# Performance work log

Hardware: AMD Instinct MI355X
Metric: run time of the kernel (lower is better)

Reference implementation:

```python
import jax, jax.numpy as jnp
import numpy as np

N = 100000   # num_nodes
E = 1600000  # num_edges
IN, HID, OUT = 128, 128, 64  # in_ft, 2*out_ft, out_ft


def setup_inputs() -> dict:
    key = jax.random.key(0)
    ks = jax.random.split(key, 8)
    x = jax.random.normal(ks[0], (N, IN), dtype=jnp.float32)
    edge_index = jax.random.randint(ks[1], (2, E), 0, N, dtype=jnp.int32)
    # Glorot-style init for GCNConv linear weights
    W1 = jax.random.normal(ks[2], (IN, HID), dtype=jnp.float32) / np.sqrt(IN).astype(np.float32)
    b1 = jnp.zeros((HID,), dtype=jnp.float32)
    W2 = jax.random.normal(ks[3], (HID, OUT), dtype=jnp.float32) / np.sqrt(HID).astype(np.float32)
    b2 = jnp.zeros((OUT,), dtype=jnp.float32)
    a = jnp.array([0.25], dtype=jnp.float32)  # shared PReLU slope (nn.PReLU default)
    return {"x": x, "edge_index": edge_index, "W1": W1, "b1": b1, "W2": W2, "b2": b2, "a": a}


def reference(x, edge_index, W1, b1, W2, b2, a):
    # PyG GCNConv semantics: add self-loops, symmetric normalization
    # norm_e = deg(src)^-1/2 * deg(dst)^-1/2, out[dst] += norm_e * (x @ W)[src] + bias
    src, dst = edge_index[0], edge_index[1]
    loops = jnp.arange(N, dtype=src.dtype)
    s = jnp.concatenate([src, loops])  # [E+N]
    d = jnp.concatenate([dst, loops])  # [E+N]
    deg = jax.ops.segment_sum(jnp.ones_like(d, dtype=x.dtype), d, num_segments=N)
    dis = jax.lax.rsqrt(deg)  # deg >= 1 thanks to self-loops
    norm = (dis[s] * dis[d])[:, None]  # [E+N, 1]

    def gcn_conv(h, W, b):
        hw = h @ W                                   # dense transform [N, F_out]
        msgs = hw[s] * norm                          # gather + scale  [E+N, F_out]
        return jax.ops.segment_sum(msgs, d, num_segments=N) + b  # scatter-add

    prelu = lambda v: jnp.where(v >= 0, v, a * v)

    h = prelu(gcn_conv(x, W1, b1))   # dropout p=0.0 -> identity
    return prelu(gcn_conv(h, W2, b2))
```

## Files before the change

### kernel.cpp

```cpp
#include <hip/hip_runtime.h>

#define N_NODES 100000
#define N_EDGES 1600000
#define BSH 9
#define NB  196
#define EPB 4096
#define CAPSH 14
#define GB  ((N_EDGES + EPB - 1) / EPB)
#define GG  ((N_NODES + 127) / 128)

typedef short bf16x8 __attribute__((ext_vector_type(8)));
typedef float f32x4 __attribute__((ext_vector_type(4)));
typedef float f32x2 __attribute__((ext_vector_type(2)));


__device__ __forceinline__ unsigned pack_bf16x2(float a, float b) {
    unsigned ua = __float_as_uint(a), ub = __float_as_uint(b);
    unsigned ra = (ua + 0x7fffu + ((ua >> 16) & 1u)) >> 16;
    unsigned rb = (ub + 0x7fffu + ((ub >> 16) & 1u)) >> 16;
    return ra | (rb << 16);
}
__device__ __forceinline__ unsigned short bf16_rne(float f) {
    unsigned u = __float_as_uint(f);
    return (unsigned short)((u + 0x7fffu + ((u >> 16) & 1u)) >> 16);
}
__device__ __forceinline__ f32x2 unpk(unsigned u) {
    f32x2 r;
    r.x = __uint_as_float(u << 16);
    r.y = __uint_as_float(u & 0xffff0000u);
    return r;
}


__device__ __forceinline__ void wt_body(const float* W, unsigned short* Wt, int C, int bid) {
    int t = bid * 256 + threadIdx.x;
    if (t >= 128 * C) return;
    int k = t / C, c = t % C;
    int g = k >> 3, j = k & 7;
    Wt[c * 128 + ((g ^ (c & 7)) << 3) + j] = bf16_rne(W[t]);
}

__global__ void setup_k(const float* __restrict__ W1, unsigned short* __restrict__ Wt1,
                        const float* __restrict__ W2, unsigned short* __restrict__ Wt2,
                        int* __restrict__ cursor) {
    int b = blockIdx.x;
    if (b < 64) { wt_body(W1, Wt1, 128, b); }
    else if (b < 96) { wt_body(W2, Wt2, 64, b - 64); }
    else {
        int t = threadIdx.x;
        if (t < NB) cursor[t] = t << CAPSH;
    }
}


__global__ __launch_bounds__(256) void bin_gemm1_k(
        const int* __restrict__ src, const int* __restrict__ dst,
        int* __restrict__ cursor, unsigned* __restrict__ binned,
        const float* __restrict__ X, const unsigned short* __restrict__ Wt,
        unsigned short* __restrict__ Y) {
    __shared__ int lhist[256];
    __shared__ int lcur[256];
    __shared__ short lds_w[128 * 128];
    int tid = threadIdx.x;

    if (blockIdx.x < GB) {
        lhist[tid] = 0;
        __syncthreads();
        int e0 = blockIdx.x * EPB;
#pragma unroll
        for (int i = 0; i < EPB / 256; ++i) {
            int e = e0 + i * 256 + tid;
            if (e < N_EDGES) atomicAdd(&lhist[dst[e] >> BSH], 1);
        }
        __syncthreads();
        {
            int c = lhist[tid];
            lcur[tid] = (tid < NB && c > 0) ? atomicAdd(&cursor[tid], c) : 0;
        }
        __syncthreads();
#pragma unroll
        for (int i = 0; i < EPB / 256; ++i) {
            int e = e0 + i * 256 + tid;
            if (e < N_EDGES) {
                int d = dst[e];
                int b = d >> BSH;
                int pos = atomicAdd(&lcur[b], 1);
                if (pos < ((b + 1) << CAPSH))
                    binned[pos] = ((unsigned)(d & ((1 << BSH) - 1)) << 17) | (unsigned)src[e];
            }
        }
        return;
    }

    {
        const uint4* srcp = (const uint4*)Wt;
        uint4* dstp = (uint4*)lds_w;
        for (int i = tid; i < 128 * 16; i += 256) dstp[i] = srcp[i];
    }
    __syncthreads();
    int lane = tid & 63;
    int r16 = lane & 15, kq = lane >> 4;
    int rbase = (blockIdx.x - GB) * 128 + (tid >> 6) * 32;
    f32x4 acc[2][8] = {};
#pragma unroll
    for (int kk = 0; kk < 4; ++kk) {
        int k0 = kk * 32 + kq * 8;
        bf16x8 a[2];
#pragma unroll
        for (int rt = 0; rt < 2; ++rt) {
            int row = rbase + rt * 16 + r16;
            if (row < N_NODES) {
                const float* xp = X + (size_t)row * 128 + k0;
                float4 f0 = *(const float4*)xp;
                float4 f1 = *(const float4*)(xp + 4);
                uint4 uu = make_uint4(pack_bf16x2(f0.x, f0.y), pack_bf16x2(f0.z, f0.w),
                                      pack_bf16x2(f1.x, f1.y), pack_bf16x2(f1.z, f1.w));
                a[rt] = *(bf16x8*)&uu;
            } else {
                bf16x8 z = {0, 0, 0, 0, 0, 0, 0, 0};
                a[rt] = z;
            }
        }
#pragma unroll
        for (int c = 0; c < 8; ++c) {
            int col = c * 16 + r16;
            int gp = (kk * 4 + kq) ^ (col & 7);
            bf16x8 b = *(const bf16x8*)&lds_w[col * 128 + gp * 8];
            acc[0][c] = __builtin_amdgcn_mfma_f32_16x16x32_bf16(a[0], b, acc[0][c], 0, 0, 0);
            acc[1][c] = __builtin_amdgcn_mfma_f32_16x16x32_bf16(a[1], b, acc[1][c], 0, 0, 0);
        }
    }
#pragma unroll
    for (int rt = 0; rt < 2; ++rt) {
#pragma unroll
        for (int c = 0; c < 8; ++c) {
#pragma unroll
            for (int r = 0; r < 4; ++r) {
                int row = rbase + rt * 16 + kq * 4 + r;
                if (row < N_NODES)
                    Y[(size_t)row * 128 + c * 16 + r16] = bf16_rne(acc[rt][c][r]);
            }
        }
    }
}

__global__ void bucket_scan_k(const int* __restrict__ cursor, int* __restrict__ bucket_base) {
    __shared__ int s[256];
    int tid = threadIdx.x;
    int v = (tid < NB) ? (cursor[tid] - (tid << CAPSH)) : 0;
    s[tid] = v; __syncthreads();
    for (int off = 1; off < 256; off <<= 1) {
        int t = 0;
        if (tid >= off) t = s[tid - off];
        __syncthreads();
        s[tid] += t;
        __syncthreads();
    }
    if (tid < NB) bucket_base[tid] = s[tid] - v;
}

__global__ __launch_bounds__(256) void deg_dis_k(const unsigned* __restrict__ binned,
                                                 const int* __restrict__ cursor,
                                                 const int* __restrict__ bucket_base,
                                                 int* __restrict__ row_start,
                                                 float* __restrict__ dis, int n, int E) {
    __shared__ int lcnt[1 << BSH];
    __shared__ int ls[256];
    int b = blockIdx.x, tid = threadIdx.x;
    for (int j = tid; j < (1 << BSH); j += 256) lcnt[j] = 0;
    __syncthreads();
    int base = b << CAPSH;
    int total = cursor[b] - base;
    for (int i = tid; i < total; i += 256)
        atomicAdd(&lcnt[binned[base + i] >> 17], 1);
    __syncthreads();
    int v0 = lcnt[2 * tid], v1 = lcnt[2 * tid + 1];
    int sv = v0 + v1;
    ls[tid] = sv;
    __syncthreads();
    for (int off = 1; off < 256; off <<= 1) {
        int t = 0;
        if (tid >= off) t = ls[tid - off];
        __syncthreads();
        ls[tid] += t;
        __syncthreads();
    }
    int pre = ls[tid] - sv;
    int nbase = b << BSH;
    int bb = bucket_base[b];
    int node0 = nbase + 2 * tid, node1 = node0 + 1;
    if (node0 < n) {
        row_start[node0] = bb + pre;
        dis[node0] = rsqrtf((float)(v0 + 1));
    }
    if (node1 < n) {
        row_start[node1] = bb + pre + v0;
        dis[node1] = rsqrtf((float)(v1 + 1));
    }
    if (b == NB - 1 && tid == 255) row_start[n] = E;
}

__global__ __launch_bounds__(256) void csr_k(const unsigned* __restrict__ binned,
                                             const int* __restrict__ cursor,
                                             const int* __restrict__ row_start,
                                             const float* __restrict__ dis,
                                             uint2* __restrict__ edge, int n) {
    __shared__ int lfill[1 << BSH];
    int b = blockIdx.x, tid = threadIdx.x;
    int nbase = b << BSH;
    for (int j = tid; j < (1 << BSH); j += 256) {
        int node = nbase + j;
        lfill[j] = (node < n) ? row_start[node] : 0;
    }
    __syncthreads();
    int base = b << CAPSH;
    int total = cursor[b] - base;
    for (int i = base + tid; i < base + total; i += 256) {
        unsigned u = binned[i];
        int s = u & 0x1FFFFu;
        int dl = u >> 17;
        int pos = atomicAdd(&lfill[dl], 1);
        edge[pos] = make_uint2((unsigned)s, __float_as_uint(dis[s] * dis[nbase + dl]));
    }
}


__global__ __launch_bounds__(256) void gemm2_k(const unsigned short* __restrict__ Xv,
                                               const unsigned short* __restrict__ Wt,
                                               unsigned short* __restrict__ Y, int nrows) {
    __shared__ short lds_w[64 * 128];
    int tid = threadIdx.x;
    {
        const uint4* srcp = (const uint4*)Wt;
        uint4* dstp = (uint4*)lds_w;
        for (int i = tid; i < 64 * 16; i += 256) dstp[i] = srcp[i];
    }
    __syncthreads();
    int lane = tid & 63;
    int r16 = lane & 15, kq = lane >> 4;
    int rbase = blockIdx.x * 128 + (tid >> 6) * 32;
    f32x4 acc[2][4] = {};
#pragma unroll
    for (int kk = 0; kk < 4; ++kk) {
        int k0 = kk * 32 + kq * 8;
        bf16x8 a[2];
#pragma unroll
        for (int rt = 0; rt < 2; ++rt) {
            int row = rbase + rt * 16 + r16;
            if (row < nrows) {
                a[rt] = *(const bf16x8*)(Xv + (size_t)row * 128 + k0);
            } else {
                bf16x8 z = {0, 0, 0, 0, 0, 0, 0, 0};
                a[rt] = z;
            }
        }
#pragma unroll
        for (int c = 0; c < 4; ++c) {
            int col = c * 16 + r16;
            int gp = (kk * 4 + kq) ^ (col & 7);
            bf16x8 b = *(const bf16x8*)&lds_w[col * 128 + gp * 8];
            acc[0][c] = __builtin_amdgcn_mfma_f32_16x16x32_bf16(a[0], b, acc[0][c], 0, 0, 0);
            acc[1][c] = __builtin_amdgcn_mfma_f32_16x16x32_bf16(a[1], b, acc[1][c], 0, 0, 0);
        }
    }
#pragma unroll
    for (int rt = 0; rt < 2; ++rt) {
#pragma unroll
        for (int c = 0; c < 4; ++c) {
#pragma unroll
            for (int r = 0; r < 4; ++r) {
                int row = rbase + rt * 16 + kq * 4 + r;
                if (row < nrows)
                    Y[(size_t)row * 64 + c * 16 + r16] = bf16_rne(acc[rt][c][r]);
            }
        }
    }
}


__global__ void agg1_k(const unsigned* __restrict__ hw, const int* __restrict__ row_start,
                       const uint2* __restrict__ edge, const float* __restrict__ dis,
                       const float* __restrict__ bias, const float* __restrict__ aslope,
                       unsigned* __restrict__ out, int n) {
    int w = (blockIdx.x * 256 + threadIdx.x) >> 6;
    int lane = threadIdx.x & 63;
    int g = lane >> 4;
    unsigned li = lane & 15;
    int node = w * 4 + g;
    bool valid = node < n;
    int e0 = valid ? row_start[node] : 0;
    int e1 = valid ? row_start[node + 1] : 0;
    unsigned rowoff = li << 4;
    const char* hwb = (const char*)hw;
    const char* edb = (const char*)edge;
    f32x2 acc[4] = {};
    int e = e0;
    while (__any(e < e1)) {
        if (e < e1) {
            uint2 ed[4];
            uint4 v[4];
#pragma unroll
            for (int u = 0; u < 4; ++u) {
                int ee = e + u;
                unsigned ec = (unsigned)((ee < e1) ? ee : (e1 - 1));
                ed[u] = *(const uint2*)(edb + (ec << 3));
            }
#pragma unroll
            for (int u = 0; u < 4; ++u)
                v[u] = *(const uint4*)(hwb + ((ed[u].x << 8) | rowoff));
#pragma unroll
            for (int u = 0; u < 4; ++u) {
                float nr = (e + u < e1) ? __uint_as_float(ed[u].y) : 0.f;
                f32x2 nr2 = {nr, nr};
                acc[0] += unpk(v[u].x) * nr2;
                acc[1] += unpk(v[u].y) * nr2;
                acc[2] += unpk(v[u].z) * nr2;
                acc[3] += unpk(v[u].w) * nr2;
            }
        }
        e += 4;
    }
    if (valid) {
        float dn = dis[node];
        f32x2 sw2 = {dn * dn, dn * dn};
        uint4 v = *(const uint4*)(hwb + (((unsigned)node << 8) | rowoff));
        acc[0] += unpk(v.x) * sw2;
        acc[1] += unpk(v.y) * sw2;
        acc[2] += unpk(v.z) * sw2;
        acc[3] += unpk(v.w) * sw2;
        float4 b0 = ((const float4*)bias)[li * 2];
        float4 b1 = ((const float4*)bias)[li * 2 + 1];
        float al = aslope[0];
        float r[8] = {acc[0].x + b0.x, acc[0].y + b0.y, acc[1].x + b0.z, acc[1].y + b0.w,
                      acc[2].x + b1.x, acc[2].y + b1.y, acc[3].x + b1.z, acc[3].y + b1.w};
#pragma unroll
        for (int j = 0; j < 8; ++j) r[j] = (r[j] >= 0.f) ? r[j] : al * r[j];
        uint4 o = make_uint4(pack_bf16x2(r[0], r[1]), pack_bf16x2(r[2], r[3]),
                             pack_bf16x2(r[4], r[5]), pack_bf16x2(r[6], r[7]));
        *(uint4*)(out + (size_t)node * 64 + li * 4) = o;
    }
}

__global__ void agg2_k(const unsigned* __restrict__ hw, const int* __restrict__ row_start,
                       const uint2* __restrict__ edge, const float* __restrict__ dis,
                       const float* __restrict__ bias, const float* __restrict__ aslope,
                       float* __restrict__ out, int n) {
    int w = (blockIdx.x * 256 + threadIdx.x) >> 6;
    int lane = threadIdx.x & 63;
    int g = lane >> 4;
    unsigned li = lane & 15;
    int node = w * 4 + g;
    bool valid = node < n;
    int e0 = valid ? row_start[node] : 0;
    int e1 = valid ? row_start[node + 1] : 0;
    unsigned rowoff = li << 3;
    const char* hwb = (const char*)hw;
    const char* edb = (const char*)edge;
    f32x2 acc[2] = {};
    int e = e0;
    while (__any(e < e1)) {
        if (e < e1) {
            uint2 ed[4];
            uint2 v[4];
#pragma unroll
            for (int u = 0; u < 4; ++u) {
                int ee = e + u;
                unsigned ec = (unsigned)((ee < e1) ? ee : (e1 - 1));
                ed[u] = *(const uint2*)(edb + (ec << 3));
            }
#pragma unroll
            for (int u = 0; u < 4; ++u)
                v[u] = *(const uint2*)(hwb + ((ed[u].x << 7) | rowoff));
#pragma unroll
            for (int u = 0; u < 4; ++u) {
                float nr = (e + u < e1) ? __uint_as_float(ed[u].y) : 0.f;
                f32x2 nr2 = {nr, nr};
                acc[0] += unpk(v[u].x) * nr2;
                acc[1] += unpk(v[u].y) * nr2;
            }
        }
        e += 4;
    }
    if (valid) {
        float dn = dis[node];
        f32x2 sw2 = {dn * dn, dn * dn};
        uint2 v = *(const uint2*)(hwb + (((unsigned)node << 7) | rowoff));
        acc[0] += unpk(v.x) * sw2;
        acc[1] += unpk(v.y) * sw2;
        float4 b = ((const float4*)bias)[li];
        float al = aslope[0];
        float r[4] = {acc[0].x + b.x, acc[0].y + b.y, acc[1].x + b.z, acc[1].y + b.w};
#pragma unroll
        for (int j = 0; j < 4; ++j) r[j] = (r[j] >= 0.f) ? r[j] : al * r[j];
        *(float4*)(out + (size_t)node * 64 + li * 4) = make_float4(r[0], r[1], r[2], r[3]);
    }
}


extern "C" void kernel_launch(void* const* d_in, const int* in_sizes, int n_in,
                              void* d_out, int out_size, void* d_ws, size_t ws_size,
                              hipStream_t stream) {
    const float* x  = (const float*)d_in[0];
    const int*   ei = (const int*)d_in[1];
    const int*   src = ei;
    const int*   dst = ei + N_EDGES;
    const float* W1 = (const float*)d_in[2];
    const float* b1 = (const float*)d_in[3];
    const float* W2 = (const float*)d_in[4];
    const float* b2 = (const float*)d_in[5];
    const float* a  = (const float*)d_in[6];
    float* out = (float*)d_out;

    char* ws = (char*)d_ws;
    size_t off = 0;
    auto alloc = [&](size_t bytes) -> void* {
        void* p = ws + off;
        off += (bytes + 255) & ~(size_t)255;
        return p;
    };
    int*            row_start = (int*)alloc((size_t)(N_NODES + 1) * 4);
    float*          dis       = (float*)alloc((size_t)N_NODES * 4);
    int*            cursor    = (int*)alloc(NB * 4);
    int*            bbase     = (int*)alloc(NB * 4);
    unsigned*       binned    = (unsigned*)alloc((size_t)NB * (1 << CAPSH) * 4);
    uint2*          edge      = (uint2*)alloc((size_t)N_EDGES * 8);
    unsigned*       hw1       = (unsigned*)alloc((size_t)N_NODES * 64 * 4);
    unsigned*       hbuf      = (unsigned*)alloc((size_t)N_NODES * 64 * 4);
    unsigned*       hw2       = (unsigned*)alloc((size_t)N_NODES * 32 * 4);
    unsigned short* Wt1       = (unsigned short*)alloc(128 * 128 * 2);
    unsigned short* Wt2       = (unsigned short*)alloc(64 * 128 * 2);

    setup_k<<<97, 256, 0, stream>>>(W1, Wt1, W2, Wt2, cursor);
    bin_gemm1_k<<<GB + GG, 256, 0, stream>>>(src, dst, cursor, binned,
                                             x, Wt1, (unsigned short*)hw1);
    bucket_scan_k<<<1, 256, 0, stream>>>(cursor, bbase);
    deg_dis_k<<<NB, 256, 0, stream>>>(binned, cursor, bbase, row_start, dis, N_NODES, N_EDGES);
    csr_k<<<NB, 256, 0, stream>>>(binned, cursor, row_start, dis, edge, N_NODES);

    int gA = (N_NODES + 1023) / 1024;
    gA = (N_NODES / 4 + 3) / 4;

    agg1_k<<<6250, 256, 0, stream>>>(hw1, row_start, edge, dis, b1, a, hbuf, N_NODES);
    gemm2_k<<<GG, 256, 0, stream>>>((unsigned short*)hbuf, Wt2, (unsigned short*)hw2, N_NODES);
    agg2_k<<<6250, 256, 0, stream>>>(hw2, row_start, edge, dis, b2, a, out, N_NODES);
    (void)gA;
}
```

Measured before the change: 186.4 us.

## Fuse layer-1 aggregation with second GEMM via LDS, unroll gathers by eight

```diff
diff --git a/kernel.cpp b/kernel.cpp
--- a/kernel.cpp
+++ b/kernel.cpp
@@ -8,6 +8,7 @@
 #define CAPSH 14
 #define GB  ((N_EDGES + EPB - 1) / EPB)
 #define GG  ((N_NODES + 127) / 128)
+#define AGB ((N_NODES + 63) / 64)
 
 typedef short bf16x8 __attribute__((ext_vector_type(8)));
 typedef float f32x4 __attribute__((ext_vector_type(4)));
@@ -225,121 +226,109 @@
 }
 
 
-__global__ __launch_bounds__(256) void gemm2_k(const unsigned short* __restrict__ Xv,
-                                               const unsigned short* __restrict__ Wt,
-                                               unsigned short* __restrict__ Y, int nrows) {
+__global__ __launch_bounds__(256) void agg1_gemm2_k(
+        const unsigned* __restrict__ hw, const int* __restrict__ row_start,
+        const uint2* __restrict__ edge, const float* __restrict__ dis,
+        const float* __restrict__ bias, const float* __restrict__ aslope,
+        const unsigned short* __restrict__ Wt2, unsigned short* __restrict__ hw2, int n) {
     __shared__ short lds_w[64 * 128];
+    __shared__ short lds_h[64 * 128];
     int tid = threadIdx.x;
     {
-        const uint4* srcp = (const uint4*)Wt;
+        const uint4* srcp = (const uint4*)Wt2;
         uint4* dstp = (uint4*)lds_w;
         for (int i = tid; i < 64 * 16; i += 256) dstp[i] = srcp[i];
     }
-    __syncthreads();
     int lane = tid & 63;
+    int g = lane >> 4;
+    unsigned li = lane & 15;
+    int wv = tid >> 6;
+    int nb0 = blockIdx.x * 64;
+    const char* hwb = (const char*)hw;
+    const char* edb = (const char*)edge;
+    float al = aslope[0];
+    float4 bb0 = ((const float4*)bias)[li * 2];
+    float4 bb1 = ((const float4*)bias)[li * 2 + 1];
+    unsigned rowoff = li << 4;
+#pragma unroll
+    for (int pass = 0; pass < 4; ++pass) {
+        int node = nb0 + wv * 16 + pass * 4 + g;
+        bool valid = node < n;
+        int e0 = valid ? row_start[node] : 0;
+        int e1 = valid ? row_start[node + 1] : 0;
+        f32x2 acc[4] = {};
+        int e = e0;
+        while (__any(e < e1)) {
+            if (e < e1) {
+                uint2 ed[8];
+                uint4 v[8];
+#pragma unroll
+                for (int u = 0; u < 8; ++u) {
+                    int ee = e + u;
+                    unsigned ec = (unsigned)((ee < e1) ? ee : (e1 - 1));
+                    ed[u] = *(const uint2*)(edb + (ec << 3));
+                }
+#pragma unroll
+                for (int u = 0; u < 8; ++u)
+                    v[u] = *(const uint4*)(hwb + ((ed[u].x << 8) | rowoff));
+#pragma unroll
+                for (int u = 0; u < 8; ++u) {
+                    float nr = (e + u < e1) ? __uint_as_float(ed[u].y) : 0.f;
+                    f32x2 nr2 = {nr, nr};
+                    acc[0] += unpk(v[u].x) * nr2;
+                    acc[1] += unpk(v[u].y) * nr2;
+                    acc[2] += unpk(v[u].z) * nr2;
+                    acc[3] += unpk(v[u].w) * nr2;
+                }
+            }
+            e += 8;
+        }
+        if (valid) {
+            float dn = dis[node];
+            f32x2 sw2 = {dn * dn, dn * dn};
+            uint4 v = *(const uint4*)(hwb + (((unsigned)node << 8) | rowoff));
+            acc[0] += unpk(v.x) * sw2;
+            acc[1] += unpk(v.y) * sw2;
+            acc[2] += unpk(v.z) * sw2;
+            acc[3] += unpk(v.w) * sw2;
+            float r[8] = {acc[0].x + bb0.x, acc[0].y + bb0.y, acc[1].x + bb0.z, acc[1].y + bb0.w,
+                          acc[2].x + bb1.x, acc[2].y + bb1.y, acc[3].x + bb1.z, acc[3].y + bb1.w};
+#pragma unroll
+            for (int j = 0; j < 8; ++j) r[j] = (r[j] >= 0.f) ? r[j] : al * r[j];
+            uint4 o = make_uint4(pack_bf16x2(r[0], r[1]), pack_bf16x2(r[2], r[3]),
+                                 pack_bf16x2(r[4], r[5]), pack_bf16x2(r[6], r[7]));
+            int lrow = node - nb0;
+            *(uint4*)((char*)lds_h + lrow * 256 + ((li ^ (unsigned)(lrow & 7)) << 4)) = o;
+        }
+    }
+    __syncthreads();
     int r16 = lane & 15, kq = lane >> 4;
-    int rbase = blockIdx.x * 128 + (tid >> 6) * 32;
-    f32x4 acc[2][4] = {};
+    int lrbase = wv * 16;
+    f32x4 acc[4] = {};
 #pragma unroll
     for (int kk = 0; kk < 4; ++kk) {
-        int k0 = kk * 32 + kq * 8;
-        bf16x8 a[2];
-#pragma unroll
-        for (int rt = 0; rt < 2; ++rt) {
-            int row = rbase + rt * 16 + r16;
-            if (row < nrows) {
-                a[rt] = *(const bf16x8*)(Xv + (size_t)row * 128 + k0);
-            } else {
-                bf16x8 z = {0, 0, 0, 0, 0, 0, 0, 0};
-                a[rt] = z;
-            }
-        }
+        int gA = kk * 4 + kq;
+        int lrow = lrbase + r16;
+        bf16x8 a = *(const bf16x8*)((const char*)lds_h + lrow * 256 + ((gA ^ (lrow & 7)) << 4));
 #pragma unroll
         for (int c = 0; c < 4; ++c) {
             int col = c * 16 + r16;
             int gp = (kk * 4 + kq) ^ (col & 7);
             bf16x8 b = *(const bf16x8*)&lds_w[col * 128 + gp * 8];
-            acc[0][c] = __builtin_amdgcn_mfma_f32_16x16x32_bf16(a[0], b, acc[0][c], 0, 0, 0);
-            acc[1][c] = __builtin_amdgcn_mfma_f32_16x16x32_bf16(a[1], b, acc[1][c], 0, 0, 0);
-        }
-    }
-#pragma unroll
-    for (int rt = 0; rt < 2; ++rt) {
-#pragma unroll
-        for (int c = 0; c < 4; ++c) {
-#pragma unroll
-            for (int r = 0; r < 4; ++r) {
-                int row = rbase + rt * 16 + kq * 4 + r;
-                if (row < nrows)
-                    Y[(size_t)row * 64 + c * 16 + r16] = bf16_rne(acc[rt][c][r]);
-            }
-        }
-    }
-}
-
-
-__global__ void agg1_k(const unsigned* __restrict__ hw, const int* __restrict__ row_start,
-                       const uint2* __restrict__ edge, const float* __restrict__ dis,
-                       const float* __restrict__ bias, const float* __restrict__ aslope,
-                       unsigned* __restrict__ out, int n) {
-    int w = (blockIdx.x * 256 + threadIdx.x) >> 6;
-    int lane = threadIdx.x & 63;
-    int g = lane >> 4;
-    unsigned li = lane & 15;
-    int node = w * 4 + g;
-    bool valid = node < n;
-    int e0 = valid ? row_start[node] : 0;
-    int e1 = valid ? row_start[node + 1] : 0;
-    unsigned rowoff = li << 4;
-    const char* hwb = (const char*)hw;
-    const char* edb = (const char*)edge;
-    f32x2 acc[4] = {};
-    int e = e0;
-    while (__any(e < e1)) {
-        if (e < e1) {
-            uint2 ed[4];
-            uint4 v[4];
-#pragma unroll
-            for (int u = 0; u < 4; ++u) {
-                int ee = e + u;
-                unsigned ec = (unsigned)((ee < e1) ? ee : (e1 - 1));
-                ed[u] = *(const uint2*)(edb + (ec << 3));
-            }
-#pragma unroll
-            for (int u = 0; u < 4; ++u)
-                v[u] = *(const uint4*)(hwb + ((ed[u].x << 8) | rowoff));
-#pragma unroll
-            for (int u = 0; u < 4; ++u) {
-                float nr = (e + u < e1) ? __uint_as_float(ed[u].y) : 0.f;
-                f32x2 nr2 = {nr, nr};
-                acc[0] += unpk(v[u].x) * nr2;
-                acc[1] += unpk(v[u].y) * nr2;
-                acc[2] += unpk(v[u].z) * nr2;
-                acc[3] += unpk(v[u].w) * nr2;
-            }
-        }
-        e += 4;
-    }
-    if (valid) {
-        float dn = dis[node];
-        f32x2 sw2 = {dn * dn, dn * dn};
-        uint4 v = *(const uint4*)(hwb + (((unsigned)node << 8) | rowoff));
-        acc[0] += unpk(v.x) * sw2;
-        acc[1] += unpk(v.y) * sw2;
-        acc[2] += unpk(v.z) * sw2;
-        acc[3] += unpk(v.w) * sw2;
-        float4 b0 = ((const float4*)bias)[li * 2];
-        float4 b1 = ((const float4*)bias)[li * 2 + 1];
-        float al = aslope[0];
-        float r[8] = {acc[0].x + b0.x, acc[0].y + b0.y, acc[1].x + b0.z, acc[1].y + b0.w,
-                      acc[2].x + b1.x, acc[2].y + b1.y, acc[3].x + b1.z, acc[3].y + b1.w};
-#pragma unroll
-        for (int j = 0; j < 8; ++j) r[j] = (r[j] >= 0.f) ? r[j] : al * r[j];
-        uint4 o = make_uint4(pack_bf16x2(r[0], r[1]), pack_bf16x2(r[2], r[3]),
-                             pack_bf16x2(r[4], r[5]), pack_bf16x2(r[6], r[7]));
-        *(uint4*)(out + (size_t)node * 64 + li * 4) = o;
-    }
-}
+            acc[c] = __builtin_amdgcn_mfma_f32_16x16x32_bf16(a, b, acc[c], 0, 0, 0);
+        }
+    }
+#pragma unroll
+    for (int c = 0; c < 4; ++c) {
+#pragma unroll
+        for (int r = 0; r < 4; ++r) {
+            int row = nb0 + lrbase + kq * 4 + r;
+            if (row < n)
+                hw2[(size_t)row * 64 + c * 16 + r16] = bf16_rne(acc[c][r]);
+        }
+    }
+}
+
 
 __global__ void agg2_k(const unsigned* __restrict__ hw, const int* __restrict__ row_start,
                        const uint2* __restrict__ edge, const float* __restrict__ dis,
@@ -360,26 +349,26 @@
     int e = e0;
     while (__any(e < e1)) {
         if (e < e1) {
-            uint2 ed[4];
-            uint2 v[4];
-#pragma unroll
-            for (int u = 0; u < 4; ++u) {
+            uint2 ed[8];
+            uint2 v[8];
+#pragma unroll
+            for (int u = 0; u < 8; ++u) {
                 int ee = e + u;
                 unsigned ec = (unsigned)((ee < e1) ? ee : (e1 - 1));
                 ed[u] = *(const uint2*)(edb + (ec << 3));
             }
 #pragma unroll
-            for (int u = 0; u < 4; ++u)
+            for (int u = 0; u < 8; ++u)
                 v[u] = *(const uint2*)(hwb + ((ed[u].x << 7) | rowoff));
 #pragma unroll
-            for (int u = 0; u < 4; ++u) {
+            for (int u = 0; u < 8; ++u) {
                 float nr = (e + u < e1) ? __uint_as_float(ed[u].y) : 0.f;
                 f32x2 nr2 = {nr, nr};
                 acc[0] += unpk(v[u].x) * nr2;
                 acc[1] += unpk(v[u].y) * nr2;
             }
         }
-        e += 4;
+        e += 8;
     }
     if (valid) {
         float dn = dis[node];
@@ -425,7 +414,6 @@
     unsigned*       binned    = (unsigned*)alloc((size_t)NB * (1 << CAPSH) * 4);
     uint2*          edge      = (uint2*)alloc((size_t)N_EDGES * 8);
     unsigned*       hw1       = (unsigned*)alloc((size_t)N_NODES * 64 * 4);
-    unsigned*       hbuf      = (unsigned*)alloc((size_t)N_NODES * 64 * 4);
     unsigned*       hw2       = (unsigned*)alloc((size_t)N_NODES * 32 * 4);
     unsigned short* Wt1       = (unsigned short*)alloc(128 * 128 * 2);
     unsigned short* Wt2       = (unsigned short*)alloc(64 * 128 * 2);
@@ -437,11 +425,7 @@
     deg_dis_k<<<NB, 256, 0, stream>>>(binned, cursor, bbase, row_start, dis, N_NODES, N_EDGES);
     csr_k<<<NB, 256, 0, stream>>>(binned, cursor, row_start, dis, edge, N_NODES);
 
-    int gA = (N_NODES + 1023) / 1024;
-    gA = (N_NODES / 4 + 3) / 4;
-
-    agg1_k<<<6250, 256, 0, stream>>>(hw1, row_start, edge, dis, b1, a, hbuf, N_NODES);
-    gemm2_k<<<GG, 256, 0, stream>>>((unsigned short*)hbuf, Wt2, (unsigned short*)hw2, N_NODES);
+    agg1_gemm2_k<<<AGB, 256, 0, stream>>>(hw1, row_start, edge, dis, b1, a,
+                                          Wt2, (unsigned short*)hw2, N_NODES);
     agg2_k<<<6250, 256, 0, stream>>>(hw2, row_start, edge, dis, b2, a, out, N_NODES);
-    (void)gA;
-}
+}
```

After: 187.7 us. Within noise of the previous version (+0.7%).

## Fuse CSR build into one kernel with padded rowranges and src-only edges

Applied to the files above, without the earlier changes.

```diff
diff --git a/kernel.cpp b/kernel.cpp
--- a/kernel.cpp
+++ b/kernel.cpp
@@ -144,26 +144,12 @@
     }
 }
 
-__global__ void bucket_scan_k(const int* __restrict__ cursor, int* __restrict__ bucket_base) {
-    __shared__ int s[256];
-    int tid = threadIdx.x;
-    int v = (tid < NB) ? (cursor[tid] - (tid << CAPSH)) : 0;
-    s[tid] = v; __syncthreads();
-    for (int off = 1; off < 256; off <<= 1) {
-        int t = 0;
-        if (tid >= off) t = s[tid - off];
-        __syncthreads();
-        s[tid] += t;
-        __syncthreads();
-    }
-    if (tid < NB) bucket_base[tid] = s[tid] - v;
-}
-
-__global__ __launch_bounds__(256) void deg_dis_k(const unsigned* __restrict__ binned,
-                                                 const int* __restrict__ cursor,
-                                                 const int* __restrict__ bucket_base,
-                                                 int* __restrict__ row_start,
-                                                 float* __restrict__ dis, int n, int E) {
+
+__global__ __launch_bounds__(256) void degcsr_k(const unsigned* __restrict__ binned,
+                                                const int* __restrict__ cursor,
+                                                int2* __restrict__ rowrange,
+                                                float* __restrict__ dis,
+                                                unsigned* __restrict__ edge, int n) {
     __shared__ int lcnt[1 << BSH];
     __shared__ int ls[256];
     int b = blockIdx.x, tid = threadIdx.x;
@@ -186,41 +172,25 @@
         __syncthreads();
     }
     int pre = ls[tid] - sv;
+    int start0 = base + pre;
+    int start1 = start0 + v0;
     int nbase = b << BSH;
-    int bb = bucket_base[b];
     int node0 = nbase + 2 * tid, node1 = node0 + 1;
     if (node0 < n) {
-        row_start[node0] = bb + pre;
+        rowrange[node0] = make_int2(start0, start0 + v0);
         dis[node0] = rsqrtf((float)(v0 + 1));
     }
     if (node1 < n) {
-        row_start[node1] = bb + pre + v0;
+        rowrange[node1] = make_int2(start1, start1 + v1);
         dis[node1] = rsqrtf((float)(v1 + 1));
     }
-    if (b == NB - 1 && tid == 255) row_start[n] = E;
-}
-
-__global__ __launch_bounds__(256) void csr_k(const unsigned* __restrict__ binned,
-                                             const int* __restrict__ cursor,
-                                             const int* __restrict__ row_start,
-                                             const float* __restrict__ dis,
-                                             uint2* __restrict__ edge, int n) {
-    __shared__ int lfill[1 << BSH];
-    int b = blockIdx.x, tid = threadIdx.x;
-    int nbase = b << BSH;
-    for (int j = tid; j < (1 << BSH); j += 256) {
-        int node = nbase + j;
-        lfill[j] = (node < n) ? row_start[node] : 0;
-    }
-    __syncthreads();
-    int base = b << CAPSH;
-    int total = cursor[b] - base;
-    for (int i = base + tid; i < base + total; i += 256) {
-        unsigned u = binned[i];
-        int s = u & 0x1FFFFu;
-        int dl = u >> 17;
-        int pos = atomicAdd(&lfill[dl], 1);
-        edge[pos] = make_uint2((unsigned)s, __float_as_uint(dis[s] * dis[nbase + dl]));
+    lcnt[2 * tid] = start0;
+    lcnt[2 * tid + 1] = start1;
+    __syncthreads();
+    for (int i = tid; i < total; i += 256) {
+        unsigned u = binned[base + i];
+        int pos = atomicAdd(&lcnt[u >> 17], 1);
+        edge[pos] = u & 0x1FFFFu;
     }
 }
 
@@ -278,8 +248,8 @@
 }
 
 
-__global__ void agg1_k(const unsigned* __restrict__ hw, const int* __restrict__ row_start,
-                       const uint2* __restrict__ edge, const float* __restrict__ dis,
+__global__ void agg1_k(const unsigned* __restrict__ hw, const int2* __restrict__ rowrange,
+                       const unsigned* __restrict__ edge, const float* __restrict__ dis,
                        const float* __restrict__ bias, const float* __restrict__ aslope,
                        unsigned* __restrict__ out, int n) {
     int w = (blockIdx.x * 256 + threadIdx.x) >> 6;
@@ -288,29 +258,31 @@
     unsigned li = lane & 15;
     int node = w * 4 + g;
     bool valid = node < n;
-    int e0 = valid ? row_start[node] : 0;
-    int e1 = valid ? row_start[node + 1] : 0;
+    int2 rr = valid ? rowrange[node] : make_int2(0, 0);
+    int e0 = rr.x, e1 = rr.y;
     unsigned rowoff = li << 4;
     const char* hwb = (const char*)hw;
-    const char* edb = (const char*)edge;
     f32x2 acc[4] = {};
     int e = e0;
     while (__any(e < e1)) {
         if (e < e1) {
-            uint2 ed[4];
+            unsigned s[4];
             uint4 v[4];
+            float wgt[4];
 #pragma unroll
             for (int u = 0; u < 4; ++u) {
                 int ee = e + u;
                 unsigned ec = (unsigned)((ee < e1) ? ee : (e1 - 1));
-                ed[u] = *(const uint2*)(edb + (ec << 3));
-            }
-#pragma unroll
-            for (int u = 0; u < 4; ++u)
-                v[u] = *(const uint4*)(hwb + ((ed[u].x << 8) | rowoff));
+                s[u] = edge[ec];
+            }
 #pragma unroll
             for (int u = 0; u < 4; ++u) {
-                float nr = (e + u < e1) ? __uint_as_float(ed[u].y) : 0.f;
+                v[u] = *(const uint4*)(hwb + ((s[u] << 8) | rowoff));
+                wgt[u] = dis[s[u]];
+            }
+#pragma unroll
+            for (int u = 0; u < 4; ++u) {
+                float nr = (e + u < e1) ? wgt[u] : 0.f;
                 f32x2 nr2 = {nr, nr};
                 acc[0] += unpk(v[u].x) * nr2;
                 acc[1] += unpk(v[u].y) * nr2;
@@ -322,17 +294,19 @@
     }
     if (valid) {
         float dn = dis[node];
-        f32x2 sw2 = {dn * dn, dn * dn};
+        f32x2 dn2 = {dn, dn};
         uint4 v = *(const uint4*)(hwb + (((unsigned)node << 8) | rowoff));
-        acc[0] += unpk(v.x) * sw2;
-        acc[1] += unpk(v.y) * sw2;
-        acc[2] += unpk(v.z) * sw2;
-        acc[3] += unpk(v.w) * sw2;
+        acc[0] += unpk(v.x) * dn2;
+        acc[1] += unpk(v.y) * dn2;
+        acc[2] += unpk(v.z) * dn2;
+        acc[3] += unpk(v.w) * dn2;
         float4 b0 = ((const float4*)bias)[li * 2];
         float4 b1 = ((const float4*)bias)[li * 2 + 1];
         float al = aslope[0];
-        float r[8] = {acc[0].x + b0.x, acc[0].y + b0.y, acc[1].x + b0.z, acc[1].y + b0.w,
-                      acc[2].x + b1.x, acc[2].y + b1.y, acc[3].x + b1.z, acc[3].y + b1.w};
+        float r[8] = {dn * acc[0].x + b0.x, dn * acc[0].y + b0.y,
+                      dn * acc[1].x + b0.z, dn * acc[1].y + b0.w,
+                      dn * acc[2].x + b1.x, dn * acc[2].y + b1.y,
+                      dn * acc[3].x + b1.z, dn * acc[3].y + b1.w};
 #pragma unroll
         for (int j = 0; j < 8; ++j) r[j] = (r[j] >= 0.f) ? r[j] : al * r[j];
         uint4 o = make_uint4(pack_bf16x2(r[0], r[1]), pack_bf16x2(r[2], r[3]),
@@ -341,8 +315,8 @@
     }
 }
 
-__global__ void agg2_k(const unsigned* __restrict__ hw, const int* __restrict__ row_start,
-                       const uint2* __restrict__ edge, const float* __restrict__ dis,
+__global__ void agg2_k(const unsigned* __restrict__ hw, const int2* __restrict__ rowrange,
+                       const unsigned* __restrict__ edge, const float* __restrict__ dis,
                        const float* __restrict__ bias, const float* __restrict__ aslope,
                        float* __restrict__ out, int n) {
     int w = (blockIdx.x * 256 + threadIdx.x) >> 6;
@@ -351,45 +325,48 @@
     unsigned li = lane & 15;
     int node = w * 4 + g;
     bool valid = node < n;
-    int e0 = valid ? row_start[node] : 0;
-    int e1 = valid ? row_start[node + 1] : 0;
+    int2 rr = valid ? rowrange[node] : make_int2(0, 0);
+    int e0 = rr.x, e1 = rr.y;
     unsigned rowoff = li << 3;
     const char* hwb = (const char*)hw;
-    const char* edb = (const char*)edge;
     f32x2 acc[2] = {};
     int e = e0;
     while (__any(e < e1)) {
         if (e < e1) {
-            uint2 ed[4];
-            uint2 v[4];
-#pragma unroll
-            for (int u = 0; u < 4; ++u) {
+            unsigned s[8];
+            uint2 v[8];
+            float wgt[8];
+#pragma unroll
+            for (int u = 0; u < 8; ++u) {
                 int ee = e + u;
                 unsigned ec = (unsigned)((ee < e1) ? ee : (e1 - 1));
-                ed[u] = *(const uint2*)(edb + (ec << 3));
-            }
-#pragma unroll
-            for (int u = 0; u < 4; ++u)
-                v[u] = *(const uint2*)(hwb + ((ed[u].x << 7) | rowoff));
-#pragma unroll
-            for (int u = 0; u < 4; ++u) {
-                float nr = (e + u < e1) ? __uint_as_float(ed[u].y) : 0.f;
+                s[u] = edge[ec];
+            }
+#pragma unroll
+            for (int u = 0; u < 8; ++u) {
+                v[u] = *(const uint2*)(hwb + ((s[u] << 7) | rowoff));
+                wgt[u] = dis[s[u]];
+            }
+#pragma unroll
+            for (int u = 0; u < 8; ++u) {
+                float nr = (e + u < e1) ? wgt[u] : 0.f;
                 f32x2 nr2 = {nr, nr};
                 acc[0] += unpk(v[u].x) * nr2;
                 acc[1] += unpk(v[u].y) * nr2;
             }
         }
-        e += 4;
+        e += 8;
     }
     if (valid) {
         float dn = dis[node];
-        f32x2 sw2 = {dn * dn, dn * dn};
+        f32x2 dn2 = {dn, dn};
         uint2 v = *(const uint2*)(hwb + (((unsigned)node << 7) | rowoff));
-        acc[0] += unpk(v.x) * sw2;
-        acc[1] += unpk(v.y) * sw2;
+        acc[0] += unpk(v.x) * dn2;
+        acc[1] += unpk(v.y) * dn2;
         float4 b = ((const float4*)bias)[li];
         float al = aslope[0];
-        float r[4] = {acc[0].x + b.x, acc[0].y + b.y, acc[1].x + b.z, acc[1].y + b.w};
+        float r[4] = {dn * acc[0].x + b.x, dn * acc[0].y + b.y,
+                      dn * acc[1].x + b.z, dn * acc[1].y + b.w};
 #pragma unroll
         for (int j = 0; j < 4; ++j) r[j] = (r[j] >= 0.f) ? r[j] : al * r[j];
         *(float4*)(out + (size_t)node * 64 + li * 4) = make_float4(r[0], r[1], r[2], r[3]);
@@ -418,12 +395,11 @@
         off += (bytes + 255) & ~(size_t)255;
         return p;
     };
-    int*            row_start = (int*)alloc((size_t)(N_NODES + 1) * 4);
+    int2*           rowrange  = (int2*)alloc((size_t)N_NODES * 8);
     float*          dis       = (float*)alloc((size_t)N_NODES * 4);
     int*            cursor    = (int*)alloc(NB * 4);
-    int*            bbase     = (int*)alloc(NB * 4);
     unsigned*       binned    = (unsigned*)alloc((size_t)NB * (1 << CAPSH) * 4);
-    uint2*          edge      = (uint2*)alloc((size_t)N_EDGES * 8);
+    unsigned*       edge      = (unsigned*)alloc((size_t)NB * (1 << CAPSH) * 4);
     unsigned*       hw1       = (unsigned*)alloc((size_t)N_NODES * 64 * 4);
     unsigned*       hbuf      = (unsigned*)alloc((size_t)N_NODES * 64 * 4);
     unsigned*       hw2       = (unsigned*)alloc((size_t)N_NODES * 32 * 4);
@@ -433,15 +409,9 @@
     setup_k<<<97, 256, 0, stream>>>(W1, Wt1, W2, Wt2, cursor);
     bin_gemm1_k<<<GB + GG, 256, 0, stream>>>(src, dst, cursor, binned,
                                              x, Wt1, (unsigned short*)hw1);
-    bucket_scan_k<<<1, 256, 0, stream>>>(cursor, bbase);
-    deg_dis_k<<<NB, 256, 0, stream>>>(binned, cursor, bbase, row_start, dis, N_NODES, N_EDGES);
-    csr_k<<<NB, 256, 0, stream>>>(binned, cursor, row_start, dis, edge, N_NODES);
-
-    int gA = (N_NODES + 1023) / 1024;
-    gA = (N_NODES / 4 + 3) / 4;
-
-    agg1_k<<<6250, 256, 0, stream>>>(hw1, row_start, edge, dis, b1, a, hbuf, N_NODES);
+    degcsr_k<<<NB, 256, 0, stream>>>(binned, cursor, rowrange, dis, edge, N_NODES);
+
+    agg1_k<<<6250, 256, 0, stream>>>(hw1, rowrange, edge, dis, b1, a, hbuf, N_NODES);
     gemm2_k<<<GG, 256, 0, stream>>>((unsigned short*)hbuf, Wt2, (unsigned short*)hw2, N_NODES);
-    agg2_k<<<6250, 256, 0, stream>>>(hw2, row_start, edge, dis, b2, a, out, N_NODES);
-    (void)gA;
-}
+    agg2_k<<<6250, 256, 0, stream>>>(hw2, rowrange, edge, dis, b2, a, out, N_NODES);
+}
```

New measurement: 174.3 us. -6.5%, faster.
